# Kernel tuning notes

Hardware: AMD Instinct MI355X
Metric: run time of the kernel (lower is better)

Reference implementation:

```python
import jax, jax.numpy as jnp
import numpy as np

NUM_NODES = 102400
NUM_EDGES = 3276800
NUM_GRAPHS = 1024
LAMBDA_MAX = 2.0


def setup_inputs() -> dict:
    key = jax.random.key(0)
    ks = jax.random.split(key, 12)
    inp = {}
    inp['x'] = jax.random.normal(ks[0], (NUM_NODES, 128), dtype=jnp.float32)
    inp['edge_index'] = jax.random.randint(ks[1], (2, NUM_EDGES), 0, NUM_NODES, dtype=jnp.int32).astype(jnp.int64)
    inp['edge_attr'] = jax.random.uniform(ks[2], (NUM_EDGES,), dtype=jnp.float32)
    inp['batch'] = jnp.sort(jax.random.randint(ks[3], (NUM_NODES,), 0, NUM_GRAPHS, dtype=jnp.int32).astype(jnp.int64))
    inp['w1'] = jax.random.normal(ks[4], (3, 128, 64), dtype=jnp.float32) * 0.05
    inp['b1'] = jax.random.normal(ks[5], (64,), dtype=jnp.float32) * 0.05
    inp['w2'] = jax.random.normal(ks[6], (3, 64, 64), dtype=jnp.float32) * 0.05
    inp['b2'] = jax.random.normal(ks[7], (64,), dtype=jnp.float32) * 0.05
    inp['w3'] = jax.random.normal(ks[8], (3, 64, 128), dtype=jnp.float32) * 0.05
    inp['b3'] = jax.random.normal(ks[9], (128,), dtype=jnp.float32) * 0.05
    inp['lin_w'] = jax.random.normal(ks[10], (128, 2), dtype=jnp.float32) * 0.05
    inp['lin_b'] = jax.random.normal(ks[11], (2,), dtype=jnp.float32) * 0.05
    return inp


def _cheb_norm(edge_index, edge_attr, num_nodes):
    # PyG ChebConv.__norm__ with normalization='sym', lambda_max=2.0:
    #   L = I - D^{-1/2} A D^{-1/2};  Lhat = (2/lambda_max) * L - I
    # off-diagonal weights: -(2/lmax) * d_i^{-1/2} w_ij d_j^{-1/2}
    # diagonal coefficient:  (2/lmax) - 1  (== 0 for lmax = 2)
    src, dst = edge_index[0], edge_index[1]
    deg = jax.ops.segment_sum(edge_attr, src, num_segments=num_nodes)
    dinv = jnp.where(deg > 0, jax.lax.rsqrt(jnp.where(deg > 0, deg, 1.0)), 0.0)
    w = -(2.0 / LAMBDA_MAX) * dinv[src] * edge_attr * dinv[dst]
    diag = (2.0 / LAMBDA_MAX) - 1.0
    return w, diag


def _cheb_conv(x, src, dst, norm_w, diag, weight, bias):
    # weight: [K, Fin, Fout]; Chebyshev recurrence T0=x, T1=Lhat x, Tk=2 Lhat T_{k-1} - T_{k-2}
    n = x.shape[0]

    def spmv(v):  # Lhat @ v via edge-list scatter/gather
        return jax.ops.segment_sum(norm_w[:, None] * v[src], dst, num_segments=n) + diag * v

    Tx0 = x
    out = Tx0 @ weight[0]
    Tx1 = spmv(Tx0)
    out = out + Tx1 @ weight[1]
    for k in range(2, weight.shape[0]):
        Tx2 = 2.0 * spmv(Tx1) - Tx0
        out = out + Tx2 @ weight[k]
        Tx0, Tx1 = Tx1, Tx2
    return out + bias


def reference(x, edge_index, edge_attr, batch, w1, b1, w2, b2, w3, b3, lin_w, lin_b):
    n = x.shape[0]
    src, dst = edge_index[0], edge_index[1]
    norm_w, diag = _cheb_norm(edge_index, edge_attr, n)
    h = jax.nn.relu(_cheb_conv(x, src, dst, norm_w, diag, w1, b1))
    h = jax.nn.relu(_cheb_conv(h, src, dst, norm_w, diag, w2, b2))
    h = jax.nn.relu(_cheb_conv(h, src, dst, norm_w, diag, w3, b3))
    # global_mean_pool over graph ids
    sums = jax.ops.segment_sum(h, batch, num_segments=NUM_GRAPHS)
    cnts = jax.ops.segment_sum(jnp.ones((n,), h.dtype), batch, num_segments=NUM_GRAPHS)
    pooled = sums / jnp.maximum(cnts, 1.0)[:, None]
    return pooled @ lin_w + lin_b
```

## Files before the change

### kernel.cpp

```cpp
#include <hip/hip_runtime.h>
#include <cstddef>
#include <cstdint>

#define N_NODES 102400
#define N_EDGES 3276800
#define N_GRAPHS 1024
#define NBUCK 400
#define NBB 1024
#define EPB 3200
#define MAXB 12288
#define N64 ((size_t)N_NODES * 64)

typedef unsigned short ushortT;
typedef unsigned int uintT;
typedef __attribute__((ext_vector_type(8))) short bf16x8;
typedef __attribute__((ext_vector_type(4))) float f32x4;

__device__ __forceinline__ float b2f(ushortT h) {
    return __uint_as_float(((uintT)h) << 16);
}
__device__ __forceinline__ ushortT f2b(float f) {
    uintT u = __float_as_uint(f);
    uintT r = (u + 0x7fffu + ((u >> 16) & 1u)) >> 16;
    return (ushortT)r;
}
__device__ __forceinline__ float loF(uintT w) { return __uint_as_float(w << 16); }
__device__ __forceinline__ float hiF(uintT w) { return __uint_as_float(w & 0xffff0000u); }

__global__ __launch_bounds__(256) void k_binA(const int* __restrict__ src,
                                              const int* __restrict__ dst,
                                              int* __restrict__ blkCntD,
                                              int* __restrict__ blkCntS) {
    __shared__ int hd[NBUCK], hs[NBUCK];
    int t = threadIdx.x;
    for (int i = t; i < NBUCK; i += 256) { hd[i] = 0; hs[i] = 0; }
    __syncthreads();
    int base = blockIdx.x * EPB;
    const int4* s4 = (const int4*)(src + base);
    const int4* d4 = (const int4*)(dst + base);
    for (int v = t; v < EPB / 4; v += 256) {
        int4 d = d4[v];
        int4 s = s4[v];
        atomicAdd(&hd[d.x >> 8], 1);
        atomicAdd(&hd[d.y >> 8], 1);
        atomicAdd(&hd[d.z >> 8], 1);
        atomicAdd(&hd[d.w >> 8], 1);
        atomicAdd(&hs[s.x >> 8], 1);
        atomicAdd(&hs[s.y >> 8], 1);
        atomicAdd(&hs[s.z >> 8], 1);
        atomicAdd(&hs[s.w >> 8], 1);
    }
    __syncthreads();
    for (int i = t; i < NBUCK; i += 256) {
        blkCntD[(size_t)blockIdx.x * NBUCK + i] = hd[i];
        blkCntS[(size_t)blockIdx.x * NBUCK + i] = hs[i];
    }
}

__global__ __launch_bounds__(512) void k_bbase(const int* __restrict__ blkCnt,
                                               int* __restrict__ blkRel,
                                               int* __restrict__ bucketTot) {
    __shared__ int sc[NBB];
    int b = blockIdx.x, t = threadIdx.x;
    int v0 = blkCnt[(size_t)t * NBUCK + b];
    int v1 = blkCnt[(size_t)(t + 512) * NBUCK + b];
    sc[t] = v0; sc[t + 512] = v1;
    __syncthreads();
    for (int o = 1; o < NBB; o <<= 1) {
        int x0 = (t >= o) ? sc[t - o] : 0;
        int x1 = (t + 512 >= o) ? sc[t + 512 - o] : 0;
        __syncthreads();
        sc[t] += x0; sc[t + 512] += x1;
        __syncthreads();
    }
    blkRel[(size_t)t * NBUCK + b] = sc[t] - v0;
    blkRel[(size_t)(t + 512) * NBUCK + b] = sc[t + 512] - v1;
    if (t == 511) bucketTot[b] = sc[NBB - 1];
}

__global__ void k_bscan(const int* __restrict__ bucketTotD,
                        const int* __restrict__ bucketTotS,
                        int* __restrict__ binBaseD,
                        int* __restrict__ binBaseS,
                        int* __restrict__ rowp) {
    int t = threadIdx.x;
    if (t == 0) {
        int run = 0;
        for (int i = 0; i < NBUCK; i++) { binBaseD[i] = run; run += bucketTotD[i]; }
        binBaseD[NBUCK] = run;
        rowp[N_NODES] = run;
    } else if (t == 64) {
        int run = 0;
        for (int i = 0; i < NBUCK; i++) { binBaseS[i] = run; run += bucketTotS[i]; }
        binBaseS[NBUCK] = run;
    }
}

__global__ __launch_bounds__(512) void k_binB2(const int* __restrict__ src,
                                               const int* __restrict__ dst,
                                               const float* __restrict__ attr,
                                               const int* __restrict__ blkCntD,
                                               const int* __restrict__ blkCntS,
                                               const int* __restrict__ blkRelD,
                                               const int* __restrict__ blkRelS,
                                               const int* __restrict__ binBaseD,
                                               const int* __restrict__ binBaseS,
                                               int2* __restrict__ edsD,
                                               int2* __restrict__ edsS) {
    __shared__ int sxD[EPB];
    __shared__ int syD[EPB];
    __shared__ ushortT spD[EPB];
    __shared__ int sxS[EPB];
    __shared__ int syS[EPB];
    __shared__ ushortT spS[EPB];
    __shared__ int lcurD[NBUCK], deltaD[NBUCK];
    __shared__ int lcurS[NBUCK], deltaS[NBUCK];
    int bx = blockIdx.x, t = threadIdx.x;

    int vD = (t < NBUCK) ? blkCntD[(size_t)bx * NBUCK + t] : 0;
    int vS = (t < NBUCK) ? blkCntS[(size_t)bx * NBUCK + t] : 0;
    sxD[t] = vD; sxS[t] = vS;
    __syncthreads();
    for (int o = 1; o < 512; o <<= 1) {
        int xD = (t >= o) ? sxD[t - o] : 0;
        int xS = (t >= o) ? sxS[t - o] : 0;
        __syncthreads();
        sxD[t] += xD; sxS[t] += xS;
        __syncthreads();
    }
    if (t < NBUCK) {
        int eD = sxD[t] - vD;
        lcurD[t] = eD;
        deltaD[t] = binBaseD[t] + blkRelD[(size_t)bx * NBUCK + t] - eD;
        int eS = sxS[t] - vS;
        lcurS[t] = eS;
        deltaS[t] = binBaseS[t] + blkRelS[(size_t)bx * NBUCK + t] - eS;
    }
    __syncthreads();

    int base = bx * EPB;
    for (int v = t; v < EPB / 2; v += 512) {
        int e0 = base + v * 2;
        int2 s2 = *(const int2*)(src + e0);
        int2 d2 = *(const int2*)(dst + e0);
        float2 a2 = *(const float2*)(attr + e0);
        int bkt, lp;
        bkt = d2.x >> 8;
        lp = atomicAdd(&lcurD[bkt], 1);
        spD[lp] = (ushortT)bkt; sxD[lp] = (s2.x << 8) | (d2.x & 255);
        syD[lp] = __float_as_int(a2.x);
        bkt = s2.x >> 8;
        lp = atomicAdd(&lcurS[bkt], 1);
        spS[lp] = (ushortT)bkt; sxS[lp] = s2.x & 255;
        syS[lp] = __float_as_int(a2.x);
        bkt = d2.y >> 8;
        lp = atomicAdd(&lcurD[bkt], 1);
        spD[lp] = (ushortT)bkt; sxD[lp] = (s2.y << 8) | (d2.y & 255);
        syD[lp] = __float_as_int(a2.y);
        bkt = s2.y >> 8;
        lp = atomicAdd(&lcurS[bkt], 1);
        spS[lp] = (ushortT)bkt; sxS[lp] = s2.y & 255;
        syS[lp] = __float_as_int(a2.y);
    }
    __syncthreads();
    for (int i = t; i < EPB; i += 512) {
        edsD[i + deltaD[spD[i]]] = make_int2(sxD[i], syD[i]);
        edsS[i + deltaS[spS[i]]] = make_int2(sxS[i], syS[i]);
    }
}

__global__ __launch_bounds__(256) void k_deg(const int2* __restrict__ edsS,
                                             const int* __restrict__ binBaseS,
                                             float* __restrict__ dinv) {
    __shared__ float degL[256];
    int b = blockIdx.x, t = threadIdx.x;
    degL[t] = 0.f;
    __syncthreads();
    int s0 = binBaseS[b], s1 = binBaseS[b + 1];
    for (int i = s0 + t; i < s1; i += 256) {
        int2 e = edsS[i];
        atomicAdd(&degL[e.x], __int_as_float(e.y));
    }
    __syncthreads();
    float d = degL[t];
    dinv[b * 256 + t] = d > 0.f ? rsqrtf(d) : 0.f;
}

__global__ __launch_bounds__(512) void k_csr(const int2* __restrict__ edsD,
                                             const int* __restrict__ binBaseD,
                                             const float* __restrict__ dinvG,
                                             int* __restrict__ rowp,
                                             int2* __restrict__ cedge) {
    __shared__ int cnt2[256 * 16];
    __shared__ int cntL[256];
    __shared__ float dL[256];
    __shared__ int2 st[MAXB];
    int b = blockIdx.x, t = threadIdx.x;
    for (int i = t; i < 256 * 16; i += 512) cnt2[i] = 0;
    if (t < 256) dL[t] = dinvG[b * 256 + t];
    __syncthreads();
    int s0 = binBaseD[b], s1 = binBaseD[b + 1];
    for (int i = s0 + t; i < s1; i += 512) {
        int2 e = edsD[i];
        atomicAdd(&cnt2[(e.x & 255) * 16 + ((e.x >> 8) >> 13)], 1);
    }
    __syncthreads();
    if (t < 256) {
        int run = 0;
#pragma unroll
        for (int o = 0; o < 16; o++) {
            int c = cnt2[t * 16 + o];
            cnt2[t * 16 + o] = run;
            run += c;
        }
        cntL[t] = run;
    }
    __syncthreads();
    int v = (t < 256) ? cntL[t] : 0;
    for (int o = 1; o < 256; o <<= 1) {
        int x = (t < 256 && t >= o) ? cntL[t - o] : 0;
        __syncthreads();
        if (t < 256) cntL[t] += x;
        __syncthreads();
    }
    if (t < 256) {
        int excl = cntL[t] - v;
        rowp[b * 256 + t] = s0 + excl;
#pragma unroll
        for (int o = 0; o < 16; o++) cnt2[t * 16 + o] += excl;
    }
    __syncthreads();
    for (int i = s0 + t; i < s1; i += 512) {
        int2 e = edsD[i];
        int dl = e.x & 255;
        int sg = e.x >> 8;
        float w = -__int_as_float(e.y) * dinvG[sg] * dL[dl];
        int p = atomicAdd(&cnt2[dl * 16 + (sg >> 13)], 1);
        st[p] = make_int2(sg, __float_as_int(w));
    }
    __syncthreads();
    int n = s1 - s0;
    for (int i = t; i < n; i += 512) cedge[s0 + i] = st[i];
}

__global__ __launch_bounds__(256) void k_cast(const float* __restrict__ x,
                                              ushortT* __restrict__ Xhi,
                                              ushortT* __restrict__ Xlo) {
    int i = blockIdx.x * 256 + threadIdx.x;
    int n = i >> 5;
    int kq = (i & 31) * 4;
    float4 v = ((const float4*)x)[i];
    int s = kq >> 6, kk = kq & 63;
    size_t o = (size_t)s * N64 + (size_t)n * 64 + kk;
    ushort4 h, l;
    h.x = f2b(v.x); l.x = f2b(v.x - b2f(h.x));
    h.y = f2b(v.y); l.y = f2b(v.y - b2f(h.y));
    h.z = f2b(v.z); l.z = f2b(v.z - b2f(h.z));
    h.w = f2b(v.w); l.w = f2b(v.w - b2f(h.w));
    *(ushort4*)(Xhi + o) = h;
    *(ushort4*)(Xlo + o) = l;
}

template <int L>
__global__ void k_wprep(const float* __restrict__ w, ushortT* __restrict__ Wth,
                        ushortT* __restrict__ Wtl) {
    int i = blockIdx.x * 256 + threadIdx.x;
    float v;
    if (L == 1) {
        if (i >= 192 * 128) return;
        int n = i / 128, k = i % 128;
        if (n < 64)       v = w[k * 64 + n] - w[16384 + k * 64 + n];
        else if (n < 128) v = w[8192 + k * 64 + (n - 64)];
        else              v = w[16384 + k * 64 + (n - 128)];
    } else if (L == 2) {
        if (i >= 192 * 64) return;
        int n = i / 64, k = i % 64;
        if (n < 64)       v = w[k * 64 + n] - w[8192 + k * 64 + n];
        else if (n < 128) v = w[4096 + k * 64 + (n - 64)];
        else              v = w[8192 + k * 64 + (n - 128)];
    } else {
        if (i >= 128 * 192) return;
        int n = i / 192, k = i % 192;
        v = w[(k >> 6) * 8192 + (k & 63) * 128 + n];
    }
    ushortT h = f2b(v);
    Wth[i] = h;
    Wtl[i] = f2b(v - b2f(h));
}

template <int KTOT, int NTOT, int MODE>
__global__ __launch_bounds__(512) void k_mgemm(
    const ushortT* __restrict__ Ah0, const ushortT* __restrict__ Ah1,
    const ushortT* __restrict__ Ah2, const ushortT* __restrict__ Al0,
    const ushortT* __restrict__ Al1, const ushortT* __restrict__ Al2,
    const ushortT* __restrict__ Wth, const ushortT* __restrict__ Wtl,
    const float* __restrict__ bias, float* __restrict__ outf,
    ushortT* __restrict__ outb, const int* __restrict__ batch,
    float* __restrict__ pooled, float* __restrict__ gcnt) {
    constexpr int KPAD = 72;
    constexpr int NCT = NTOT / 16;
    constexpr int SMEM_STAGE = 2 * NTOT * KPAD * 2;
    constexpr int SMEM_POOL = (MODE == 1) ? (256 * 128 * 4 + 256 * 4) : 0;
    constexpr int SMEM_BYTES = SMEM_STAGE > SMEM_POOL ? SMEM_STAGE : SMEM_POOL;
    __shared__ __align__(16) char smem[SMEM_BYTES];
    ushortT* Bh = (ushortT*)smem;
    ushortT* Bl = Bh + NTOT * KPAD;
    const ushortT* Ah[3] = {Ah0, Ah1, Ah2};
    const ushortT* Al[3] = {Al0, Al1, Al2};
    int t = threadIdx.x;
    int lane = t & 63;
    int wv = t >> 6;
    int m = lane & 15, q = lane >> 4;
    int r0 = blockIdx.x * 256 + wv * 32;
    int ar0 = r0 + m;
    int ar1 = r0 + 16 + m;

    f32x4 acc[2][NCT];
#pragma unroll
    for (int rf = 0; rf < 2; rf++)
#pragma unroll
        for (int ct = 0; ct < NCT; ct++)
#pragma unroll
            for (int j = 0; j < 4; j++) acc[rf][ct][j] = 0.f;

#pragma unroll
    for (int kc = 0; kc < KTOT / 64; kc++) {
        __syncthreads();
        for (int i = t; i < NTOT * 8; i += 512) {
            int col = i >> 3, k = (i & 7) * 8;
            *(uint4*)(Bh + col * KPAD + k) =
                *(const uint4*)(Wth + (size_t)col * KTOT + kc * 64 + k);
            *(uint4*)(Bl + col * KPAD + k) =
                *(const uint4*)(Wtl + (size_t)col * KTOT + kc * 64 + k);
        }
        __syncthreads();
        const ushortT* Ahc = Ah[kc];
        const ushortT* Alc = Al[kc];
#pragma unroll
        for (int ks2 = 0; ks2 < 2; ks2++) {
            int kk = ks2 * 32 + q * 8;
            bf16x8 ah0 = *(const bf16x8*)(Ahc + (size_t)ar0 * 64 + kk);
            bf16x8 al0 = *(const bf16x8*)(Alc + (size_t)ar0 * 64 + kk);
            bf16x8 ah1 = *(const bf16x8*)(Ahc + (size_t)ar1 * 64 + kk);
            bf16x8 al1 = *(const bf16x8*)(Alc + (size_t)ar1 * 64 + kk);
#pragma unroll
            for (int ct = 0; ct < NCT; ct++) {
                int bo = (ct * 16 + m) * KPAD + ks2 * 32 + q * 8;
                bf16x8 bh = *(const bf16x8*)(Bh + bo);
                bf16x8 bl = *(const bf16x8*)(Bl + bo);
                acc[0][ct] = __builtin_amdgcn_mfma_f32_16x16x32_bf16(ah0, bh, acc[0][ct], 0, 0, 0);
                acc[0][ct] = __builtin_amdgcn_mfma_f32_16x16x32_bf16(al0, bh, acc[0][ct], 0, 0, 0);
                acc[0][ct] = __builtin_amdgcn_mfma_f32_16x16x32_bf16(ah0, bl, acc[0][ct], 0, 0, 0);
                acc[1][ct] = __builtin_amdgcn_mfma_f32_16x16x32_bf16(ah1, bh, acc[1][ct], 0, 0, 0);
                acc[1][ct] = __builtin_amdgcn_mfma_f32_16x16x32_bf16(al1, bh, acc[1][ct], 0, 0, 0);
                acc[1][ct] = __builtin_amdgcn_mfma_f32_16x16x32_bf16(ah1, bl, acc[1][ct], 0, 0, 0);
            }
        }
    }

    if (MODE == 0) {
#pragma unroll
        for (int rf = 0; rf < 2; rf++)
#pragma unroll
            for (int ct = 0; ct < NCT; ct++)
#pragma unroll
                for (int rg = 0; rg < 4; rg++) {
                    int row = r0 + rf * 16 + q * 4 + rg;
                    float v = acc[rf][ct][rg];
                    if (ct < 8)
                        outf[(size_t)row * 128 + ct * 16 + m] = v;
                    else
                        outb[(size_t)row * 64 + (ct - 8) * 16 + m] = f2b(v);
                }
    } else {
        float* poolB = (float*)smem;
        int* batchL = (int*)(smem + 256 * 128 * 4);
        __syncthreads();
        for (int i = t; i < 256; i += 512)
            batchL[i] = batch[blockIdx.x * 256 + i];
#pragma unroll
        for (int rf = 0; rf < 2; rf++)
#pragma unroll
            for (int ct = 0; ct < NCT; ct++)
#pragma unroll
                for (int rg = 0; rg < 4; rg++) {
                    int rl = wv * 32 + rf * 16 + q * 4 + rg;
                    int col = ct * 16 + m;
                    poolB[rl * 128 + col] = fmaxf(acc[rf][ct][rg] + bias[col], 0.f);
                }
        __syncthreads();
        int col = t & 127, seg = t >> 7;
        int base = seg * 64;
        int g = batchL[base];
        float a = 0.f;
        int c = 0;
        for (int k = 0; k < 64; k++) {
            int gn = batchL[base + k];
            if (gn != g) {
                atomicAdd(&pooled[(size_t)g * 128 + col], a);
                if (col == 0) atomicAdd(&gcnt[g], (float)c);
                g = gn; a = 0.f; c = 0;
            }
            a += poolB[(base + k) * 128 + col];
            c++;
        }
        atomicAdd(&pooled[(size_t)g * 128 + col], a);
        if (col == 0) atomicAdd(&gcnt[g], (float)c);
    }
}

template <int MODE, int SA, bool AUXB, bool WLO>
__global__ __launch_bounds__(256) void k_spmm(const int* __restrict__ rowp,
                                              const int2* __restrict__ cedge,
                                              const ushortT* __restrict__ Xb,
                                              const float* __restrict__ auxF,
                                              const ushortT* __restrict__ auxH,
                                              const ushortT* __restrict__ auxL,
                                              const float* __restrict__ bias,
                                              ushortT* __restrict__ Yh,
                                              ushortT* __restrict__ Yl) {
    int node = blockIdx.x * 4 + (threadIdx.x >> 6);
    int lane = threadIdx.x & 63;
    int q = lane >> 3;
    int f = (lane & 7) * 8;
    int s = rowp[node], e = rowp[node + 1];
    const ushortT* Xf = Xb + f;
    float a0 = 0.f, a1 = 0.f, a2 = 0.f, a3 = 0.f;
    float a4 = 0.f, a5 = 0.f, a6 = 0.f, a7 = 0.f;
    for (int i = s; i < e; i += 16) {
        int i0 = min(i + q, e - 1);
        int i1 = min(i + 8 + q, e - 1);
        int2 ed0 = cedge[i0];
        int2 ed1 = cedge[i1];
        float w0 = (i + q < e) ? __int_as_float(ed0.y) : 0.f;
        float w1 = (i + 8 + q < e) ? __int_as_float(ed1.y) : 0.f;
        uint4 u0 = *(const uint4*)(Xf + ((size_t)ed0.x << 6));
        uint4 u1 = *(const uint4*)(Xf + ((size_t)ed1.x << 6));
        a0 = fmaf(w0, loF(u0.x), a0);
        a1 = fmaf(w0, hiF(u0.x), a1);
        a2 = fmaf(w0, loF(u0.y), a2);
        a3 = fmaf(w0, hiF(u0.y), a3);
        a4 = fmaf(w0, loF(u0.z), a4);
        a5 = fmaf(w0, hiF(u0.z), a5);
        a6 = fmaf(w0, loF(u0.w), a6);
        a7 = fmaf(w0, hiF(u0.w), a7);
        a0 = fmaf(w1, loF(u1.x), a0);
        a1 = fmaf(w1, hiF(u1.x), a1);
        a2 = fmaf(w1, loF(u1.y), a2);
        a3 = fmaf(w1, hiF(u1.y), a3);
        a4 = fmaf(w1, loF(u1.z), a4);
        a5 = fmaf(w1, hiF(u1.z), a5);
        a6 = fmaf(w1, loF(u1.w), a6);
        a7 = fmaf(w1, hiF(u1.w), a7);
    }
    a0 += __shfl_xor(a0, 8); a0 += __shfl_xor(a0, 16); a0 += __shfl_xor(a0, 32);
    a1 += __shfl_xor(a1, 8); a1 += __shfl_xor(a1, 16); a1 += __shfl_xor(a1, 32);
    a2 += __shfl_xor(a2, 8); a2 += __shfl_xor(a2, 16); a2 += __shfl_xor(a2, 32);
    a3 += __shfl_xor(a3, 8); a3 += __shfl_xor(a3, 16); a3 += __shfl_xor(a3, 32);
    a4 += __shfl_xor(a4, 8); a4 += __shfl_xor(a4, 16); a4 += __shfl_xor(a4, 32);
    a5 += __shfl_xor(a5, 8); a5 += __shfl_xor(a5, 16); a5 += __shfl_xor(a5, 32);
    a6 += __shfl_xor(a6, 8); a6 += __shfl_xor(a6, 16); a6 += __shfl_xor(a6, 32);
    a7 += __shfl_xor(a7, 8); a7 += __shfl_xor(a7, 16); a7 += __shfl_xor(a7, 32);

    if (q == 0 || (WLO && q == 1)) {
        float x0 = 0.f, x1 = 0.f, x2 = 0.f, x3 = 0.f;
        float x4 = 0.f, x5 = 0.f, x6 = 0.f, x7 = 0.f;
        if (MODE != 0) {
            if (AUXB) {
                uint4 ha = *(const uint4*)(auxH + (size_t)node * 64 + f);
                uint4 la = *(const uint4*)(auxL + (size_t)node * 64 + f);
                x0 = loF(ha.x) + loF(la.x);
                x1 = hiF(ha.x) + hiF(la.x);
                x2 = loF(ha.y) + loF(la.y);
                x3 = hiF(ha.y) + hiF(la.y);
                x4 = loF(ha.z) + loF(la.z);
                x5 = hiF(ha.z) + hiF(la.z);
                x6 = loF(ha.w) + loF(la.w);
                x7 = hiF(ha.w) + hiF(la.w);
            } else {
                float4 av0 = *(const float4*)(auxF + (size_t)node * SA + f);
                float4 av1 = *(const float4*)(auxF + (size_t)node * SA + f + 4);
                x0 = av0.x; x1 = av0.y; x2 = av0.z; x3 = av0.w;
                x4 = av1.x; x5 = av1.y; x6 = av1.z; x7 = av1.w;
            }
        }
        float r0, r1, r2, r3, r4, r5, r6, r7;
        if (MODE == 0) {
            r0 = a0; r1 = a1; r2 = a2; r3 = a3;
            r4 = a4; r5 = a5; r6 = a6; r7 = a7;
        } else if (MODE == 1) {
            r0 = x0 + 2.f * a0; r1 = x1 + 2.f * a1;
            r2 = x2 + 2.f * a2; r3 = x3 + 2.f * a3;
            r4 = x4 + 2.f * a4; r5 = x5 + 2.f * a5;
            r6 = x6 + 2.f * a6; r7 = x7 + 2.f * a7;
        } else if (MODE == 2) {
            r0 = 2.f * a0 - x0; r1 = 2.f * a1 - x1;
            r2 = 2.f * a2 - x2; r3 = 2.f * a3 - x3;
            r4 = 2.f * a4 - x4; r5 = 2.f * a5 - x5;
            r6 = 2.f * a6 - x6; r7 = 2.f * a7 - x7;
        } else {
            float4 bv0 = *(const float4*)(bias + f);
            float4 bv1 = *(const float4*)(bias + f + 4);
            r0 = fmaxf(x0 + a0 + bv0.x, 0.f);
            r1 = fmaxf(x1 + a1 + bv0.y, 0.f);
            r2 = fmaxf(x2 + a2 + bv0.z, 0.f);
            r3 = fmaxf(x3 + a3 + bv0.w, 0.f);
            r4 = fmaxf(x4 + a4 + bv1.x, 0.f);
            r5 = fmaxf(x5 + a5 + bv1.y, 0.f);
            r6 = fmaxf(x6 + a6 + bv1.z, 0.f);
            r7 = fmaxf(x7 + a7 + bv1.w, 0.f);
        }
        ushortT h0 = f2b(r0), h1 = f2b(r1), h2 = f2b(r2), h3 = f2b(r3);
        ushortT h4 = f2b(r4), h5 = f2b(r5), h6 = f2b(r6), h7 = f2b(r7);
        if (q == 0) {
            uint4 pk;
            pk.x = (uintT)h0 | ((uintT)h1 << 16);
            pk.y = (uintT)h2 | ((uintT)h3 << 16);
            pk.z = (uintT)h4 | ((uintT)h5 << 16);
            pk.w = (uintT)h6 | ((uintT)h7 << 16);
            *(uint4*)(Yh + (size_t)node * 64 + f) = pk;
        } else {
            uint4 pk;
            pk.x = (uintT)f2b(r0 - b2f(h0)) | ((uintT)f2b(r1 - b2f(h1)) << 16);
            pk.y = (uintT)f2b(r2 - b2f(h2)) | ((uintT)f2b(r3 - b2f(h3)) << 16);
            pk.z = (uintT)f2b(r4 - b2f(h4)) | ((uintT)f2b(r5 - b2f(h5)) << 16);
            pk.w = (uintT)f2b(r6 - b2f(h6)) | ((uintT)f2b(r7 - b2f(h7)) << 16);
            *(uint4*)(Yl + (size_t)node * 64 + f) = pk;
        }
    }
}

__global__ void k_final(const float* __restrict__ pooled, const float* __restrict__ gcnt,
                        const float* __restrict__ lin_w, const float* __restrict__ lin_b,
                        float* __restrict__ out) {
    int g = blockIdx.x * 4 + (threadIdx.x >> 6);
    int lane = threadIdx.x & 63;
    if (g >= N_GRAPHS) return;
    float inv = 1.f / fmaxf(gcnt[g], 1.f);
    float v0 = pooled[(size_t)g * 128 + lane] * inv;
    float v1 = pooled[(size_t)g * 128 + 64 + lane] * inv;
    float p0 = v0 * lin_w[lane * 2 + 0] + v1 * lin_w[(lane + 64) * 2 + 0];
    float p1 = v0 * lin_w[lane * 2 + 1] + v1 * lin_w[(lane + 64) * 2 + 1];
    for (int o = 32; o > 0; o >>= 1) {
        p0 += __shfl_down(p0, o);
        p1 += __shfl_down(p1, o);
    }
    if (lane == 0) {
        out[g * 2 + 0] = p0 + lin_b[0];
        out[g * 2 + 1] = p1 + lin_b[1];
    }
}

extern "C" void kernel_launch(void* const* d_in, const int* in_sizes, int n_in,
                              void* d_out, int out_size, void* d_ws, size_t ws_size,
                              hipStream_t stream) {
    const float* x     = (const float*)d_in[0];
    const int*   src   = (const int*)d_in[1];
    const int*   dst   = src + N_EDGES;
    const float* eattr = (const float*)d_in[2];
    const int*   batch = (const int*)d_in[3];
    const float* w1    = (const float*)d_in[4];
    const float* b1    = (const float*)d_in[5];
    const float* w2    = (const float*)d_in[6];
    const float* b2    = (const float*)d_in[7];
    const float* w3    = (const float*)d_in[8];
    const float* b3    = (const float*)d_in[9];
    const float* lin_w = (const float*)d_in[10];
    const float* lin_b = (const float*)d_in[11];
    float* out = (float*)d_out;

    char* ws = (char*)d_ws;
    size_t off = 0;
    auto alloc = [&](size_t bytes) -> char* {
        char* p = ws + off;
        off += (bytes + 255) & ~(size_t)255;
        return p;
    };
    int*   blkCntD   = (int*)  alloc((size_t)NBB * NBUCK * 4);
    int*   blkCntS   = (int*)  alloc((size_t)NBB * NBUCK * 4);
    int*   blkRelD   = (int*)  alloc((size_t)NBB * NBUCK * 4);
    int*   blkRelS   = (int*)  alloc((size_t)NBB * NBUCK * 4);
    int*   bucketTotD = (int*) alloc(NBUCK * 4);
    int*   bucketTotS = (int*) alloc(NBUCK * 4);
    int*   binBaseD  = (int*)  alloc((NBUCK + 1) * 4);
    int*   binBaseS  = (int*)  alloc((NBUCK + 1) * 4);
    float* dinv      = (float*)alloc((size_t)N_NODES * 4);
    int*   rowp      = (int*)  alloc((size_t)(N_NODES + 1) * 4);
    ushortT* Wt1h   = (ushortT*)alloc(192 * 128 * 2);
    ushortT* Wt1l   = (ushortT*)alloc(192 * 128 * 2);
    ushortT* Wt2h   = (ushortT*)alloc(192 * 64 * 2);
    ushortT* Wt2l   = (ushortT*)alloc(192 * 64 * 2);
    ushortT* Wt3h   = (ushortT*)alloc(128 * 192 * 2);
    ushortT* Wt3l   = (ushortT*)alloc(128 * 192 * 2);
    float* pooled   = (float*)alloc((size_t)(N_GRAPHS * 128 + N_GRAPHS) * 4);
    float* gcnt     = pooled + (size_t)N_GRAPHS * 128;
    int2*  cedge    = (int2*) alloc((size_t)N_EDGES * 8);
    char*  Buf1     = alloc((size_t)N_EDGES * 16);
    char*  Buf2     = alloc((size_t)N_NODES * 128 * 4);
    char*  Buf3     = alloc(4 * N64 * 2);

    int2* edsD = (int2*)Buf1;
    int2* edsS = edsD + N_EDGES;
    ushortT* Xhi  = (ushortT*)Buf1;
    ushortT* Xlo  = Xhi + 2 * N64;
    ushortT* GThi = (ushortT*)Buf1;
    float* P  = (float*)Buf2;
    ushortT* G0    = (ushortT*)Buf3;
    ushortT* Qhi   = G0 + N64;
    ushortT* H1hi  = G0 + 2 * N64;
    ushortT* H1lo  = G0 + 3 * N64;
    ushortT* GTlo0 = G0;
    ushortT* GTlo1 = H1hi;
    ushortT* GTlo2 = H1lo;

    hipMemsetAsync(pooled, 0, (size_t)(N_GRAPHS * 128 + N_GRAPHS) * 4, stream);

    k_binA<<<NBB, 256, 0, stream>>>(src, dst, blkCntD, blkCntS);
    k_bbase<<<NBUCK, 512, 0, stream>>>(blkCntD, blkRelD, bucketTotD);
    k_bbase<<<NBUCK, 512, 0, stream>>>(blkCntS, blkRelS, bucketTotS);
    k_bscan<<<1, 128, 0, stream>>>(bucketTotD, bucketTotS, binBaseD, binBaseS, rowp);
    k_binB2<<<NBB, 512, 0, stream>>>(src, dst, eattr, blkCntD, blkCntS,
                                     blkRelD, blkRelS, binBaseD, binBaseS,
                                     edsD, edsS);
    k_deg<<<NBUCK, 256, 0, stream>>>(edsS, binBaseS, dinv);
    k_csr<<<NBUCK, 512, 0, stream>>>(edsD, binBaseD, dinv, rowp, cedge);

    k_cast<<<N_NODES * 32 / 256, 256, 0, stream>>>(x, Xhi, Xlo);
    k_wprep<1><<<96, 256, 0, stream>>>(w1, Wt1h, Wt1l);
    k_wprep<2><<<48, 256, 0, stream>>>(w2, Wt2h, Wt2l);
    k_wprep<3><<<96, 256, 0, stream>>>(w3, Wt3h, Wt3l);

    k_mgemm<128, 192, 0><<<N_NODES / 256, 512, 0, stream>>>(
        Xhi, Xhi + N64, nullptr, Xlo, Xlo + N64, nullptr, Wt1h, Wt1l, nullptr,
        P, G0, nullptr, nullptr, nullptr);
    k_spmm<1, 128, false, false><<<N_NODES / 4, 256, 0, stream>>>(
        rowp, cedge, G0, P + 64, nullptr, nullptr, nullptr, Qhi, nullptr);
    k_spmm<3, 128, false, true><<<N_NODES / 4, 256, 0, stream>>>(
        rowp, cedge, Qhi, P, nullptr, nullptr, b1, H1hi, H1lo);

    k_mgemm<64, 192, 0><<<N_NODES / 256, 512, 0, stream>>>(
        H1hi, nullptr, nullptr, H1lo, nullptr, nullptr, Wt2h, Wt2l, nullptr,
        P, G0, nullptr, nullptr, nullptr);
    k_spmm<1, 128, false, false><<<N_NODES / 4, 256, 0, stream>>>(
        rowp, cedge, G0, P + 64, nullptr, nullptr, nullptr, Qhi, nullptr);
    k_spmm<3, 128, false, true><<<N_NODES / 4, 256, 0, stream>>>(
        rowp, cedge, Qhi, P, nullptr, nullptr, b2, GThi, GTlo0);

    k_spmm<0, 64, false, true><<<N_NODES / 4, 256, 0, stream>>>(
        rowp, cedge, GThi, nullptr, nullptr, nullptr, nullptr, GThi + N64, GTlo1);
    k_spmm<2, 64, true, true><<<N_NODES / 4, 256, 0, stream>>>(
        rowp, cedge, GThi + N64, nullptr, GThi, GTlo0, nullptr, GThi + 2 * N64, GTlo2);
    k_mgemm<192, 128, 1><<<N_NODES / 256, 512, 0, stream>>>(
        GThi, GThi + N64, GThi + 2 * N64, GTlo0, GTlo1, GTlo2, Wt3h, Wt3l, b3,
        nullptr, nullptr, batch, pooled, gcnt);

    k_final<<<N_GRAPHS / 4, 256, 0, stream>>>(pooled, gcnt, lin_w, lin_b, out);
}
```

Measured before the change: 727.4 us.

## Transpose bin counts, parallelize bucket scan, simplify CSR build, merge weight prep

The per-block bucket counts are transposed through an LDS tile so the per-bucket scan kernel reads them with coalesced loads instead of strided ones. The single-thread serial bucket scan becomes a 512-thread parallel scan. The CSR build drops its 16-way sub-bucket sort and shared-memory staging and scatters edges straight to global memory via per-row atomic cursors. Three weight-prep launches are merged into one. The CSR change gives up the within-row ordering by source, which may hurt gather locality in the SpMM kernels, and the transpose adds a kernel launch plus extra buffers.

```diff
diff --git a/kernel.cpp b/kernel.cpp
--- a/kernel.cpp
+++ b/kernel.cpp
@@ -8,7 +8,6 @@
 #define NBUCK 400
 #define NBB 1024
 #define EPB 3200
-#define MAXB 12288
 #define N64 ((size_t)N_NODES * 64)
 
 typedef unsigned short ushortT;
@@ -57,13 +56,32 @@
     }
 }
 
-__global__ __launch_bounds__(512) void k_bbase(const int* __restrict__ blkCnt,
+__global__ void k_tr(const int* __restrict__ inD, const int* __restrict__ inS,
+                     int* __restrict__ outD, int* __restrict__ outS) {
+    __shared__ int tile[32][33];
+    const int* in = blockIdx.z ? inS : inD;
+    int* out = blockIdx.z ? outS : outD;
+    int x = blockIdx.x * 32 + threadIdx.x;
+    int yb = blockIdx.y * 32;
+    for (int dy = threadIdx.y; dy < 32; dy += 8) {
+        int y = yb + dy;
+        tile[dy][threadIdx.x] = (x < NBUCK) ? in[(size_t)y * NBUCK + x] : 0;
+    }
+    __syncthreads();
+    int xo = yb + threadIdx.x;
+    for (int dy = threadIdx.y; dy < 32; dy += 8) {
+        int bo = blockIdx.x * 32 + dy;
+        if (bo < NBUCK) out[(size_t)bo * NBB + xo] = tile[threadIdx.x][dy];
+    }
+}
+
+__global__ __launch_bounds__(512) void k_bbase(const int* __restrict__ blkCntT,
                                                int* __restrict__ blkRel,
                                                int* __restrict__ bucketTot) {
     __shared__ int sc[NBB];
     int b = blockIdx.x, t = threadIdx.x;
-    int v0 = blkCnt[(size_t)t * NBUCK + b];
-    int v1 = blkCnt[(size_t)(t + 512) * NBUCK + b];
+    int v0 = blkCntT[(size_t)b * NBB + t];
+    int v1 = blkCntT[(size_t)b * NBB + t + 512];
     sc[t] = v0; sc[t + 512] = v1;
     __syncthreads();
     for (int o = 1; o < NBB; o <<= 1) {
@@ -78,22 +96,36 @@
     if (t == 511) bucketTot[b] = sc[NBB - 1];
 }
 
-__global__ void k_bscan(const int* __restrict__ bucketTotD,
-                        const int* __restrict__ bucketTotS,
-                        int* __restrict__ binBaseD,
-                        int* __restrict__ binBaseS,
-                        int* __restrict__ rowp) {
+__global__ __launch_bounds__(512) void k_bscan(const int* __restrict__ bucketTotD,
+                                               const int* __restrict__ bucketTotS,
+                                               int* __restrict__ binBaseD,
+                                               int* __restrict__ binBaseS,
+                                               int* __restrict__ rowp) {
+    __shared__ int sc[512];
     int t = threadIdx.x;
-    if (t == 0) {
-        int run = 0;
-        for (int i = 0; i < NBUCK; i++) { binBaseD[i] = run; run += bucketTotD[i]; }
-        binBaseD[NBUCK] = run;
-        rowp[N_NODES] = run;
-    } else if (t == 64) {
-        int run = 0;
-        for (int i = 0; i < NBUCK; i++) { binBaseS[i] = run; run += bucketTotS[i]; }
-        binBaseS[NBUCK] = run;
-    }
+    int vD = (t < NBUCK) ? bucketTotD[t] : 0;
+    sc[t] = vD;
+    __syncthreads();
+    for (int o = 1; o < 512; o <<= 1) {
+        int x = (t >= o) ? sc[t - o] : 0;
+        __syncthreads();
+        sc[t] += x;
+        __syncthreads();
+    }
+    if (t < NBUCK) binBaseD[t] = sc[t] - vD;
+    if (t == 511) { binBaseD[NBUCK] = sc[511]; rowp[N_NODES] = sc[511]; }
+    __syncthreads();
+    int vS = (t < NBUCK) ? bucketTotS[t] : 0;
+    sc[t] = vS;
+    __syncthreads();
+    for (int o = 1; o < 512; o <<= 1) {
+        int x = (t >= o) ? sc[t - o] : 0;
+        __syncthreads();
+        sc[t] += x;
+        __syncthreads();
+    }
+    if (t < NBUCK) binBaseS[t] = sc[t] - vS;
+    if (t == 511) binBaseS[NBUCK] = sc[511];
 }
 
 __global__ __launch_bounds__(512) void k_binB2(const int* __restrict__ src,
@@ -191,29 +223,15 @@
                                              const float* __restrict__ dinvG,
                                              int* __restrict__ rowp,
                                              int2* __restrict__ cedge) {
-    __shared__ int cnt2[256 * 16];
     __shared__ int cntL[256];
+    __shared__ int curL[256];
     __shared__ float dL[256];
-    __shared__ int2 st[MAXB];
     int b = blockIdx.x, t = threadIdx.x;
-    for (int i = t; i < 256 * 16; i += 512) cnt2[i] = 0;
-    if (t < 256) dL[t] = dinvG[b * 256 + t];
+    if (t < 256) { cntL[t] = 0; dL[t] = dinvG[b * 256 + t]; }
     __syncthreads();
     int s0 = binBaseD[b], s1 = binBaseD[b + 1];
     for (int i = s0 + t; i < s1; i += 512) {
-        int2 e = edsD[i];
-        atomicAdd(&cnt2[(e.x & 255) * 16 + ((e.x >> 8) >> 13)], 1);
-    }
-    __syncthreads();
-    if (t < 256) {
-        int run = 0;
-#pragma unroll
-        for (int o = 0; o < 16; o++) {
-            int c = cnt2[t * 16 + o];
-            cnt2[t * 16 + o] = run;
-            run += c;
-        }
-        cntL[t] = run;
+        atomicAdd(&cntL[edsD[i].x & 255], 1);
     }
     __syncthreads();
     int v = (t < 256) ? cntL[t] : 0;
@@ -225,9 +243,8 @@
     }
     if (t < 256) {
         int excl = cntL[t] - v;
+        curL[t] = s0 + excl;
         rowp[b * 256 + t] = s0 + excl;
-#pragma unroll
-        for (int o = 0; o < 16; o++) cnt2[t * 16 + o] += excl;
     }
     __syncthreads();
     for (int i = s0 + t; i < s1; i += 512) {
@@ -235,12 +252,9 @@
         int dl = e.x & 255;
         int sg = e.x >> 8;
         float w = -__int_as_float(e.y) * dinvG[sg] * dL[dl];
-        int p = atomicAdd(&cnt2[dl * 16 + (sg >> 13)], 1);
-        st[p] = make_int2(sg, __float_as_int(w));
-    }
-    __syncthreads();
-    int n = s1 - s0;
-    for (int i = t; i < n; i += 512) cedge[s0 + i] = st[i];
+        int p = atomicAdd(&curL[dl], 1);
+        cedge[p] = make_int2(sg, __float_as_int(w));
+    }
 }
 
 __global__ __launch_bounds__(256) void k_cast(const float* __restrict__ x,
@@ -261,31 +275,42 @@
     *(ushort4*)(Xlo + o) = l;
 }
 
-template <int L>
-__global__ void k_wprep(const float* __restrict__ w, ushortT* __restrict__ Wth,
-                        ushortT* __restrict__ Wtl) {
-    int i = blockIdx.x * 256 + threadIdx.x;
+__global__ void k_wprepAll(const float* __restrict__ w1f,
+                           const float* __restrict__ w2f,
+                           const float* __restrict__ w3f,
+                           ushortT* __restrict__ Wt1h, ushortT* __restrict__ Wt1l,
+                           ushortT* __restrict__ Wt2h, ushortT* __restrict__ Wt2l,
+                           ushortT* __restrict__ Wt3h, ushortT* __restrict__ Wt3l) {
+    int bid = blockIdx.x;
     float v;
-    if (L == 1) {
-        if (i >= 192 * 128) return;
+    if (bid < 96) {
+        int i = bid * 256 + threadIdx.x;
         int n = i / 128, k = i % 128;
+        const float* w = w1f;
         if (n < 64)       v = w[k * 64 + n] - w[16384 + k * 64 + n];
         else if (n < 128) v = w[8192 + k * 64 + (n - 64)];
         else              v = w[16384 + k * 64 + (n - 128)];
-    } else if (L == 2) {
-        if (i >= 192 * 64) return;
+        ushortT h = f2b(v);
+        Wt1h[i] = h;
+        Wt1l[i] = f2b(v - b2f(h));
+    } else if (bid < 144) {
+        int i = (bid - 96) * 256 + threadIdx.x;
         int n = i / 64, k = i % 64;
+        const float* w = w2f;
         if (n < 64)       v = w[k * 64 + n] - w[8192 + k * 64 + n];
         else if (n < 128) v = w[4096 + k * 64 + (n - 64)];
         else              v = w[8192 + k * 64 + (n - 128)];
+        ushortT h = f2b(v);
+        Wt2h[i] = h;
+        Wt2l[i] = f2b(v - b2f(h));
     } else {
-        if (i >= 128 * 192) return;
+        int i = (bid - 144) * 256 + threadIdx.x;
         int n = i / 192, k = i % 192;
-        v = w[(k >> 6) * 8192 + (k & 63) * 128 + n];
-    }
-    ushortT h = f2b(v);
-    Wth[i] = h;
-    Wtl[i] = f2b(v - b2f(h));
+        v = w3f[(k >> 6) * 8192 + (k & 63) * 128 + n];
+        ushortT h = f2b(v);
+        Wt3h[i] = h;
+        Wt3l[i] = f2b(v - b2f(h));
+    }
 }
 
 template <int KTOT, int NTOT, int MODE>
@@ -578,6 +603,8 @@
     };
     int*   blkCntD   = (int*)  alloc((size_t)NBB * NBUCK * 4);
     int*   blkCntS   = (int*)  alloc((size_t)NBB * NBUCK * 4);
+    int*   blkCntDT  = (int*)  alloc((size_t)NBUCK * NBB * 4);
+    int*   blkCntST  = (int*)  alloc((size_t)NBUCK * NBB * 4);
     int*   blkRelD   = (int*)  alloc((size_t)NBB * NBUCK * 4);
     int*   blkRelS   = (int*)  alloc((size_t)NBB * NBUCK * 4);
     int*   bucketTotD = (int*) alloc(NBUCK * 4);
@@ -616,9 +643,11 @@
     hipMemsetAsync(pooled, 0, (size_t)(N_GRAPHS * 128 + N_GRAPHS) * 4, stream);
 
     k_binA<<<NBB, 256, 0, stream>>>(src, dst, blkCntD, blkCntS);
-    k_bbase<<<NBUCK, 512, 0, stream>>>(blkCntD, blkRelD, bucketTotD);
-    k_bbase<<<NBUCK, 512, 0, stream>>>(blkCntS, blkRelS, bucketTotS);
-    k_bscan<<<1, 128, 0, stream>>>(bucketTotD, bucketTotS, binBaseD, binBaseS, rowp);
+    k_tr<<<dim3(13, 32, 2), dim3(32, 8), 0, stream>>>(blkCntD, blkCntS,
+                                                      blkCntDT, blkCntST);
+    k_bbase<<<NBUCK, 512, 0, stream>>>(blkCntDT, blkRelD, bucketTotD);
+    k_bbase<<<NBUCK, 512, 0, stream>>>(blkCntST, blkRelS, bucketTotS);
+    k_bscan<<<1, 512, 0, stream>>>(bucketTotD, bucketTotS, binBaseD, binBaseS, rowp);
     k_binB2<<<NBB, 512, 0, stream>>>(src, dst, eattr, blkCntD, blkCntS,
                                      blkRelD, blkRelS, binBaseD, binBaseS,
                                      edsD, edsS);
@@ -626,9 +655,8 @@
     k_csr<<<NBUCK, 512, 0, stream>>>(edsD, binBaseD, dinv, rowp, cedge);
 
     k_cast<<<N_NODES * 32 / 256, 256, 0, stream>>>(x, Xhi, Xlo);
-    k_wprep<1><<<96, 256, 0, stream>>>(w1, Wt1h, Wt1l);
-    k_wprep<2><<<48, 256, 0, stream>>>(w2, Wt2h, Wt2l);
-    k_wprep<3><<<96, 256, 0, stream>>>(w3, Wt3h, Wt3l);
+    k_wprepAll<<<240, 256, 0, stream>>>(w1, w2, w3, Wt1h, Wt1l, Wt2h, Wt2l,
+                                        Wt3h, Wt3l);
 
     k_mgemm<128, 192, 0><<<N_NODES / 256, 512, 0, stream>>>(
         Xhi, Xhi + N64, nullptr, Xlo, Xlo + N64, nullptr, Wt1h, Wt1l, nullptr,
```

New measurement: 715.0 us, median of 2. About the same (-1.7%).
